# Optimization experiments

Measured on AMD Instinct MI355X. Metric: run time of the kernel, lower is better.

The kernel has to match this reference:

```python
import jax, jax.numpy as jnp
import numpy as np

DIM = 768
HEADS = 12
DIM_HEAD = 64
INNER = HEADS * DIM_HEAD  # 768
B, N = 8, 1024


def layernorm(x, gamma, beta, eps=1e-5):
    mu = jnp.mean(x, axis=-1, keepdims=True)
    var = jnp.var(x, axis=-1, keepdims=True)
    return (x - mu) * jax.lax.rsqrt(var + eps) * gamma + beta


def setup_inputs() -> dict:
    key = jax.random.key(0)
    ks = jax.random.split(key, 12)
    s = lambda fan_in: 1.0 / np.sqrt(fan_in)
    return {
        "x": jax.random.normal(ks[0], (B, N, DIM), dtype=jnp.float32),
        "ln1_g": jnp.ones((DIM,), jnp.float32),
        "ln1_b": jnp.zeros((DIM,), jnp.float32),
        "ln2_g": jnp.ones((DIM,), jnp.float32),
        "ln2_b": jnp.zeros((DIM,), jnp.float32),
        "w_qkv": jax.random.uniform(ks[1], (DIM, 3 * INNER), jnp.float32, -s(DIM), s(DIM)),
        "w_out": jax.random.uniform(ks[2], (INNER, DIM), jnp.float32, -s(INNER), s(INNER)),
        "b_out": jax.random.uniform(ks[3], (DIM,), jnp.float32, -s(INNER), s(INNER)),
        "w_ff1": jax.random.uniform(ks[4], (DIM, 4 * DIM), jnp.float32, -s(DIM), s(DIM)),
        "b_ff1": jax.random.uniform(ks[5], (4 * DIM,), jnp.float32, -s(DIM), s(DIM)),
        "w_ff2": jax.random.uniform(ks[6], (4 * DIM, DIM), jnp.float32, -s(4 * DIM), s(4 * DIM)),
        "b_ff2": jax.random.uniform(ks[7], (DIM,), jnp.float32, -s(4 * DIM), s(4 * DIM)),
    }


def reference(x, ln1_g, ln1_b, ln2_g, ln2_b, w_qkv, w_out, b_out, w_ff1, b_ff1, w_ff2, b_ff2):
    # --- attention sub-block (dropout = identity, eval mode) ---
    residual = x
    h = layernorm(x, ln1_g, ln1_b)
    qkv = h @ w_qkv  # [B, N, 3*INNER]
    q, k, v = jnp.split(qkv, 3, axis=-1)
    # b n (h d) -> b h n d
    reshape = lambda t: t.reshape(B, N, HEADS, DIM_HEAD).transpose(0, 2, 1, 3)
    q, k, v = reshape(q), reshape(k), reshape(v)
    scale = DIM_HEAD ** -0.5
    attn = jnp.einsum('bhnd,bhmd->bhnm', q, k) * scale
    attn = jax.nn.softmax(attn, axis=-1)
    out = jnp.einsum('bhnm,bhmd->bhnd', attn, v)
    out = out.transpose(0, 2, 1, 3).reshape(B, N, INNER)  # b h n d -> b n (h d)
    out = out @ w_out + b_out
    x = residual + out
    # --- FFN sub-block ---
    h2 = layernorm(x, ln2_g, ln2_b)
    ff = jax.nn.gelu(h2 @ w_ff1 + b_ff1, approximate=False) @ w_ff2 + b_ff2
    return x + ff
```

## Files before the change

kernel.cpp:

```cpp
#include <hip/hip_runtime.h>
#include <hip/hip_bf16.h>
#include <math.h>
#include <stdint.h>

#define BATCH 8
#define SEQ   1024
#define DIM   768
#define HEADS 12
#define DHEAD 64
#define TOK   (BATCH*SEQ)
#define INNER 768
#define FFDIM 3072
#define QKVN  2304
#define QKLD  1536

typedef float floatx4 __attribute__((ext_vector_type(4)));
typedef __bf16 bf16x8 __attribute__((ext_vector_type(8)));

__device__ __forceinline__ float b2f(uint16_t u) {
    return __uint_as_float(((uint32_t)u) << 16);
}
__device__ __forceinline__ uint16_t f2b(float f) {
    uint32_t x = __float_as_uint(f);
    x += 0x7fffu + ((x >> 16) & 1u);
    return (uint16_t)(x >> 16);
}
__device__ __forceinline__ uint32_t cvt_pk_bf16(float lo, float hi) {
    uint32_t r;
    asm("v_cvt_pk_bf16_f32 %0, %1, %2" : "=v"(r) : "v"(lo), "v"(hi));
    return r;
}
__device__ __forceinline__ float exp2_fast(float x) {
    float r; asm("v_exp_f32 %0, %1" : "=v"(r) : "v"(x)); return r;
}
__device__ __forceinline__ float rcp_fast(float x) {
    float r; asm("v_rcp_f32 %0, %1" : "=v"(r) : "v"(x)); return r;
}

__device__ __forceinline__ float gelu_exact(float v) {
    float x  = v * 0.70710678f;
    float ax = fabsf(x);
    float t  = rcp_fast(fmaf(0.3275911f, ax, 1.0f));
    float poly = t * fmaf(t, fmaf(t, fmaf(t, fmaf(t, 1.061405429f, -1.453152027f),
                          1.421413741f), -0.284496736f), 0.254829592f);
    float e = 1.0f - poly * exp2_fast(x * x * -1.44269504f);
    float erfv = copysignf(e, x);
    return 0.5f * v * (1.0f + erfv);
}

__global__ __launch_bounds__(256) void transpose_all(
    const float* __restrict__ w_qkv, const float* __restrict__ w_out,
    const float* __restrict__ w_ff1, const float* __restrict__ w_ff2,
    uint16_t* __restrict__ WqT, uint16_t* __restrict__ WoT,
    uint16_t* __restrict__ W1T, uint16_t* __restrict__ W2T)
{
    __shared__ float tile[32][33];
    int bid = blockIdx.x;
    const float* in; uint16_t* outp; int R, C, tx, ty;
    if (bid < 1728)      { in = w_qkv; outp = WqT; R = 768;  C = 2304; tx = bid % 72;            ty = bid / 72; }
    else if (bid < 2304) { int q = bid - 1728; in = w_out; outp = WoT; R = 768;  C = 768;  tx = q % 24; ty = q / 24; }
    else if (bid < 4608) { int q = bid - 2304; in = w_ff1; outp = W1T; R = 768;  C = 3072; tx = q % 96; ty = q / 96; }
    else                 { int q = bid - 4608; in = w_ff2; outp = W2T; R = 3072; C = 768;  tx = q % 24; ty = q / 24; }
    int c0 = tx * 32, r0 = ty * 32;
    int x = threadIdx.x;
    int y = threadIdx.y;
    #pragma unroll
    for (int i = y; i < 32; i += 8)
        tile[i][x] = in[(size_t)(r0 + i) * C + c0 + x];
    __syncthreads();
    #pragma unroll
    for (int i = y; i < 32; i += 8)
        outp[(size_t)(c0 + i) * R + r0 + x] = f2b(tile[x][i]);
}

__global__ __launch_bounds__(256) void ln_naive(
    const float* __restrict__ x, const float* __restrict__ g,
    const float* __restrict__ be, uint16_t* __restrict__ y)
{
    const int lane = threadIdx.x & 63;
    const size_t row = blockIdx.x * 4 + (threadIdx.x >> 6);
    float v[12];
    float s = 0.f, ss = 0.f;
    #pragma unroll
    for (int j = 0; j < 12; j++) {
        int idx = lane + j * 64;
        float f = x[row * DIM + idx];
        v[j] = f; s += f; ss += f * f;
    }
    #pragma unroll
    for (int off = 32; off > 0; off >>= 1) {
        s  += __shfl_xor(s, off);
        ss += __shfl_xor(ss, off);
    }
    const float mu = s * (1.f / DIM);
    const float var = ss * (1.f / DIM) - mu * mu;
    const float rstd = rsqrtf(var + 1e-5f);
    #pragma unroll
    for (int j = 0; j < 12; j++) {
        int idx = lane + j * 64;
        y[row * DIM + idx] = f2b((v[j] - mu) * rstd * g[idx] + be[idx]);
    }
}

template<bool BIAS, bool GELU, bool RES, bool OUTF, bool VSPLIT>
__global__ __launch_bounds__(256) void gemm_bt(
    const uint16_t* __restrict__ A, const uint16_t* __restrict__ Bt,
    void* C, const float* __restrict__ bias, int bias_off,
    const float* res, int N, int K, int lda, int ldbt, int ldc,
    uint16_t* __restrict__ vt)
{
    __shared__ __align__(16) uint16_t a_s[2][128 * 32];
    __shared__ __align__(16) uint16_t b_s[2][128 * 32];
    const int tid = threadIdx.x;
    const int wave = tid >> 6, lane = tid & 63;
    const int wr = wave >> 1, wc = wave & 1;

    const int nwg = gridDim.x * gridDim.y;
    int bid = blockIdx.y * gridDim.x + blockIdx.x;
    if ((nwg & 7) == 0)
        bid = (bid & 7) * (nwg >> 3) + (bid >> 3);
    const int tileM = (bid / gridDim.x) * 128;
    const int tileN = (bid % gridDim.x) * 128;

    floatx4 acc[4][4] = {};

    const int scol = (tid & 3) * 8;
    const int srow = tid >> 2;
    const int lm = lane & 15;
    const int lq = lane >> 4;
    const int kq = lq * 8;

    const uint16_t* Ab0 = A  + (size_t)(tileM + srow) * lda;
    const uint16_t* Ab1 = A  + (size_t)(tileM + 64 + srow) * lda;
    const uint16_t* Bb0 = Bt + (size_t)(tileN + srow) * ldbt;
    const uint16_t* Bb1 = Bt + (size_t)(tileN + 64 + srow) * ldbt;

    const int nt = K >> 5;

    uint4 ar0, ar1, br0, br1;
    ar0 = *(const uint4*)(Ab0 + scol);
    ar1 = *(const uint4*)(Ab1 + scol);
    br0 = *(const uint4*)(Bb0 + scol);
    br1 = *(const uint4*)(Bb1 + scol);
    *(uint4*)&a_s[0][srow * 32 + scol]        = ar0;
    *(uint4*)&a_s[0][(64 + srow) * 32 + scol] = ar1;
    *(uint4*)&b_s[0][srow * 32 + scol]        = br0;
    *(uint4*)&b_s[0][(64 + srow) * 32 + scol] = br1;

    int cur = 0;
    for (int t = 0; t < nt; ++t) {
        __syncthreads();

        if (t + 1 < nt) {
            const int kk = (t + 1) * 32 + scol;
            ar0 = *(const uint4*)(Ab0 + kk);
            ar1 = *(const uint4*)(Ab1 + kk);
            br0 = *(const uint4*)(Bb0 + kk);
            br1 = *(const uint4*)(Bb1 + kk);
        }

        bf16x8 af[4], bfr[4];
        #pragma unroll
        for (int rt = 0; rt < 4; rt++) {
            int r = wr * 64 + rt * 16 + lm;
            af[rt] = *(const bf16x8*)&a_s[cur][r * 32 + kq];
        }
        #pragma unroll
        for (int ntt = 0; ntt < 4; ntt++) {
            int n = wc * 64 + ntt * 16 + lm;
            bfr[ntt] = *(const bf16x8*)&b_s[cur][n * 32 + kq];
        }
        #pragma unroll
        for (int rt = 0; rt < 4; rt++)
            #pragma unroll
            for (int ntt = 0; ntt < 4; ntt++)
                acc[rt][ntt] = __builtin_amdgcn_mfma_f32_16x16x32_bf16(
                    af[rt], bfr[ntt], acc[rt][ntt], 0, 0, 0);

        if (t + 1 < nt) {
            *(uint4*)&a_s[cur ^ 1][srow * 32 + scol]        = ar0;
            *(uint4*)&a_s[cur ^ 1][(64 + srow) * 32 + scol] = ar1;
            *(uint4*)&b_s[cur ^ 1][srow * 32 + scol]        = br0;
            *(uint4*)&b_s[cur ^ 1][(64 + srow) * 32 + scol] = br1;
        }
        cur ^= 1;
    }

    const bool vpath = VSPLIT && (tileN >= 1536);
    #pragma unroll
    for (int rt = 0; rt < 4; rt++) {
        int r0 = tileM + wr * 64 + rt * 16 + lq * 4;
        #pragma unroll
        for (int ntt = 0; ntt < 4; ntt++) {
            int cg = tileN + wc * 64 + ntt * 16 + lm;
            if (vpath) {
                int d = cg - 1536;
                int bb = r0 >> 10, s0 = r0 & 1023;
                uint32_t p0 = (uint32_t)f2b(acc[rt][ntt][0]) | ((uint32_t)f2b(acc[rt][ntt][1]) << 16);
                uint32_t p1 = (uint32_t)f2b(acc[rt][ntt][2]) | ((uint32_t)f2b(acc[rt][ntt][3]) << 16);
                uint2 pk; pk.x = p0; pk.y = p1;
                *(uint2*)&vt[((size_t)bb * 768 + d) * 1024 + s0] = pk;
            } else {
                float bvv = BIAS ? bias[bias_off + cg] : 0.f;
                #pragma unroll
                for (int r = 0; r < 4; r++) {
                    float v = acc[rt][ntt][r] + bvv;
                    if (GELU) v = gelu_exact(v);
                    size_t ci = (size_t)(r0 + r) * ldc + cg;
                    if (RES) v += res[ci];
                    if (OUTF) ((float*)C)[ci] = v;
                    else      ((uint16_t*)C)[ci] = f2b(v);
                }
            }
        }
    }
}

#define KSWZ(row, cb) ((cb) ^ (((row) & 7) << 4))
#define NKT (SEQ / 64)
#define SM_C   0.18033688f
#define SM_THR 11.5416f

__global__ __launch_bounds__(512) void flash_mfma(
    uint16_t* qk, const uint16_t* __restrict__ vt)
{
    __shared__ __align__(16) uint16_t k_s[2][64 * 64];
    __shared__ __align__(16) uint16_t v_s[2][64 * 64];
    __shared__ __align__(16) uint16_t p_s[128 * 64];
    char* k_base = (char*)k_s;
    char* v_base = (char*)v_s;
    char* p_c    = (char*)p_s;

    const int t = threadIdx.x;
    const int wq = t >> 6;
    const int lane = t & 63;
    const int lm = lane & 15;
    const int lq = lane >> 4;

    int flat = blockIdx.x + 8 * (blockIdx.y + 12 * blockIdx.z);
    int nw = (flat & 7) * 96 + (flat >> 3);
    const int b   = nw / 96;
    const int rem = nw - b * 96;
    const int h   = rem >> 3;
    const int qb  = rem & 7;

    const size_t rowbase = (size_t)b * SEQ;
    const int hcol = h * DHEAD;

    bf16x8 qf[2];
    {
        const uint16_t* qp = qk + (rowbase + qb*128 + wq*16 + lm) * QKLD + hcol + lq*8;
        qf[0] = *(const bf16x8*)qp;
        qf[1] = *(const bf16x8*)(qp + 32);
    }

    floatx4 O[4] = {};
    float m_q = -1e30f, l_q = 0.f;

    const int s_row = t >> 3;
    const int s_cb  = (t & 7) * 16;
    const size_t kgbase = (rowbase + s_row) * QKLD + INNER + hcol;
    const size_t vgbase = ((size_t)b * 768 + hcol + s_row) * 1024;

    uint4 kr0, vr0;
    {
        kr0 = *(const uint4*)((const char*)(qk + kgbase) + s_cb);
        vr0 = *(const uint4*)((const char*)(vt + vgbase) + s_cb);
        *(uint4*)&k_base[s_row*128 + KSWZ(s_row, s_cb)] = kr0;
        *(uint4*)&v_base[s_row*128 + KSWZ(s_row, s_cb)] = vr0;
    }

    int cur = 0;
    for (int kt = 0; kt < NKT; ++kt) {
        __syncthreads();

        if (kt + 1 < NKT) {
            kr0 = *(const uint4*)((const char*)(qk + kgbase + (size_t)(kt + 1) * 64 * QKLD) + s_cb);
            vr0 = *(const uint4*)((const char*)(vt + vgbase + (size_t)(kt + 1) * 64) + s_cb);
        }

        const char* k_c = k_base + cur * 8192;
        const char* v_c = v_base + cur * 8192;

        floatx4 S[4];
        __builtin_amdgcn_s_setprio(1);
        #pragma unroll
        for (int nt = 0; nt < 4; nt++) {
            const int row = nt*16 + lm;
            bf16x8 ak0 = *(const bf16x8*)&k_c[row*128 + KSWZ(row, lq*16)];
            bf16x8 ak1 = *(const bf16x8*)&k_c[row*128 + KSWZ(row, 64 + lq*16)];
            floatx4 a = {};
            a = __builtin_amdgcn_mfma_f32_16x16x32_bf16(ak0, qf[0], a, 0, 0, 0);
            a = __builtin_amdgcn_mfma_f32_16x16x32_bf16(ak1, qf[1], a, 0, 0, 0);
            S[nt] = a;
        }
        __builtin_amdgcn_s_setprio(0);

        float m0 = fmaxf(fmaxf(S[0][0], S[0][1]), fmaxf(S[0][2], S[0][3]));
        float m1 = fmaxf(fmaxf(S[1][0], S[1][1]), fmaxf(S[1][2], S[1][3]));
        float m2 = fmaxf(fmaxf(S[2][0], S[2][1]), fmaxf(S[2][2], S[2][3]));
        float m3 = fmaxf(fmaxf(S[3][0], S[3][1]), fmaxf(S[3][2], S[3][3]));
        float mx = fmaxf(fmaxf(m0, m1), fmaxf(m2, m3)) * SM_C;
        mx = fmaxf(mx, __shfl_xor(mx, 16));
        mx = fmaxf(mx, __shfl_xor(mx, 32));

        float mn = m_q;
        if (!__all(mx <= m_q + SM_THR)) {
            mn = fmaxf(m_q, mx);
            float alpha = exp2_fast(m_q - mn);
            m_q = mn;
            l_q *= alpha;
            #pragma unroll
            for (int nt = 0; nt < 4; nt++) {
                O[nt][0] *= alpha; O[nt][1] *= alpha;
                O[nt][2] *= alpha; O[nt][3] *= alpha;
            }
        }

        float p[4][4];
        float sum = 0.f;
        #pragma unroll
        for (int nt = 0; nt < 4; nt++) {
            float p0 = exp2_fast(fmaf(S[nt][0], SM_C, -mn));
            float p1 = exp2_fast(fmaf(S[nt][1], SM_C, -mn));
            float p2 = exp2_fast(fmaf(S[nt][2], SM_C, -mn));
            float p3 = exp2_fast(fmaf(S[nt][3], SM_C, -mn));
            p[nt][0] = p0; p[nt][1] = p1; p[nt][2] = p2; p[nt][3] = p3;
            sum += (p0 + p1) + (p2 + p3);
        }
        sum += __shfl_xor(sum, 16);
        sum += __shfl_xor(sum, 32);
        l_q += sum;

        const int prow = wq*16 + lm;
        #pragma unroll
        for (int nt = 0; nt < 4; nt++) {
            uint2 w;
            w.x = cvt_pk_bf16(p[nt][0], p[nt][1]);
            w.y = cvt_pk_bf16(p[nt][2], p[nt][3]);
            *(uint2*)&p_c[prow*128 + KSWZ(prow, nt*32 + lq*8)] = w;
        }

        __builtin_amdgcn_s_setprio(1);
        #pragma unroll
        for (int ks = 0; ks < 2; ks++) {
            bf16x8 bp = *(const bf16x8*)&p_c[prow*128 + KSWZ(prow, ks*64 + lq*16)];
            #pragma unroll
            for (int nt = 0; nt < 4; nt++) {
                const int vrow = nt*16 + lm;
                bf16x8 av = *(const bf16x8*)&v_c[vrow*128 + KSWZ(vrow, ks*64 + lq*16)];
                O[nt] = __builtin_amdgcn_mfma_f32_16x16x32_bf16(av, bp, O[nt], 0, 0, 0);
            }
        }
        __builtin_amdgcn_s_setprio(0);

        if (kt + 1 < NKT) {
            char* kn = k_base + (cur ^ 1) * 8192;
            char* vn = v_base + (cur ^ 1) * 8192;
            *(uint4*)&kn[s_row*128 + KSWZ(s_row, s_cb)] = kr0;
            *(uint4*)&vn[s_row*128 + KSWZ(s_row, s_cb)] = vr0;
        }
        cur ^= 1;
    }

    const float linv = rcp_fast(l_q);
    uint16_t* dst = qk + (rowbase + qb*128 + wq*16 + lm) * QKLD + hcol;
    #pragma unroll
    for (int nt = 0; nt < 4; nt++) {
        uint2 w;
        w.x = cvt_pk_bf16(O[nt][0] * linv, O[nt][1] * linv);
        w.y = cvt_pk_bf16(O[nt][2] * linv, O[nt][3] * linv);
        *(uint2*)&dst[nt*16 + lq*4] = w;
    }
}

extern "C" void kernel_launch(void* const* d_in, const int* in_sizes, int n_in,
                              void* d_out, int out_size, void* d_ws, size_t ws_size,
                              hipStream_t stream) {
    const float* x      = (const float*)d_in[0];
    const float* ln1_g  = (const float*)d_in[1];
    const float* ln1_b  = (const float*)d_in[2];
    const float* ln2_g  = (const float*)d_in[3];
    const float* ln2_b  = (const float*)d_in[4];
    const float* w_qkv  = (const float*)d_in[5];
    const float* w_out  = (const float*)d_in[6];
    const float* b_out  = (const float*)d_in[7];
    const float* w_ff1  = (const float*)d_in[8];
    const float* b_ff1  = (const float*)d_in[9];
    const float* w_ff2  = (const float*)d_in[10];
    const float* b_ff2  = (const float*)d_in[11];
    float* out = (float*)d_out;

    uint16_t* ws  = (uint16_t*)d_ws;
    uint16_t* qk  = ws;
    uint16_t* ffc = ws;
    uint16_t* vT  = ws + (size_t)12582912;
    uint16_t* h   = ws + (size_t)18874368;
    uint16_t* WqT = ws + (size_t)25165824;
    uint16_t* WoT = ws + (size_t)26935296;
    uint16_t* W1T = ws + (size_t)27525120;
    uint16_t* W2T = ws + (size_t)29884416;

    hipLaunchKernelGGL(transpose_all, dim3(6912), dim3(32, 8), 0, stream,
                       w_qkv, w_out, w_ff1, w_ff2, WqT, WoT, W1T, W2T);

    hipLaunchKernelGGL(ln_naive, dim3(TOK/4), dim3(256), 0, stream, x, ln1_g, ln1_b, h);
    hipLaunchKernelGGL((gemm_bt<false, false, false, false, true>), dim3(QKVN/128, TOK/128), dim3(256), 0, stream,
                       h, WqT, qk, nullptr, 0, nullptr, QKVN, DIM, DIM, DIM, QKLD, vT);
    hipLaunchKernelGGL(flash_mfma, dim3(SEQ/128, HEADS, BATCH), dim3(512), 0, stream, qk, vT);
    hipLaunchKernelGGL((gemm_bt<true, false, true, true, false>), dim3(DIM/128, TOK/128), dim3(256), 0, stream,
                       qk, WoT, out, b_out, 0, x, DIM, INNER, QKLD, DIM, DIM, nullptr);
    hipLaunchKernelGGL(ln_naive, dim3(TOK/4), dim3(256), 0, stream, out, ln2_g, ln2_b, h);
    for (int c = 0; c < 2; c++) {
        hipLaunchKernelGGL((gemm_bt<true, true, false, false, false>), dim3(1536/128, TOK/128), dim3(256), 0, stream,
                           h, W1T + (size_t)c*1536*DIM, ffc, b_ff1, c*1536, nullptr,
                           1536, DIM, DIM, DIM, 1536, nullptr);
        if (c == 0) {
            hipLaunchKernelGGL((gemm_bt<true, false, true, true, false>), dim3(DIM/128, TOK/128), dim3(256), 0, stream,
                               ffc, W2T + (size_t)c*1536, out, b_ff2, 0, out,
                               DIM, 1536, 1536, FFDIM, DIM, nullptr);
        } else {
            hipLaunchKernelGGL((gemm_bt<false, false, true, true, false>), dim3(DIM/128, TOK/128), dim3(256), 0, stream,
                               ffc, W2T + (size_t)c*1536, out, nullptr, 0, out,
                               DIM, 1536, 1536, FFDIM, DIM, nullptr);
        }
    }
}
```

Before: 403.1 us.

## Add 256x256-tile GEMM kernel for QKV and FF1 projections

Introduces a new 512-thread GEMM with 256x256 output tiles, register-prefetched double-buffered LDS, and an XCD-aware block remap. It is used for the QKV projection (including the V-transpose epilogue) and the FF1+GELU GEMMs. Larger tiles raise arithmetic intensity and reduce redundant global loads of A and B. In exchange each thread holds a 128-float accumulator, which raises register pressure and may limit occupancy. The grids also shrink (QKV goes to 288 blocks, FF1 to 192), so the 256 CUs may be unevenly loaded.

Result: slower. 417.3 us (+3.5%).

```diff
diff --git a/kernel.cpp b/kernel.cpp
--- a/kernel.cpp
+++ b/kernel.cpp
@@ -216,6 +216,119 @@
     }
 }
 
+template<bool BIAS, bool GELU, bool VSPLIT>
+__global__ __launch_bounds__(512, 2) void gemm_bt256(
+    const uint16_t* __restrict__ A, const uint16_t* __restrict__ Bt,
+    void* C, const float* __restrict__ bias, int bias_off,
+    int K, int lda, int ldbt, int ldc,
+    uint16_t* __restrict__ vt)
+{
+    __shared__ __align__(16) uint16_t a_s[2][256 * 32];
+    __shared__ __align__(16) uint16_t b_s[2][256 * 32];
+    const int tid = threadIdx.x;
+    const int wave = tid >> 6, lane = tid & 63;
+    const int wr = wave >> 2;
+    const int wc = wave & 3;
+
+    const int nwg = gridDim.x * gridDim.y;
+    int bid = blockIdx.y * gridDim.x + blockIdx.x;
+    if ((nwg & 7) == 0)
+        bid = (bid & 7) * (nwg >> 3) + (bid >> 3);
+    const int tileM = (bid / gridDim.x) * 256;
+    const int tileN = (bid % gridDim.x) * 256;
+
+    floatx4 acc[8][4] = {};
+
+    const int scol = (tid & 3) * 8;
+    const int srow = tid >> 2;
+    const int lm = lane & 15;
+    const int lq = lane >> 4;
+    const int kq = lq * 8;
+
+    const uint16_t* Ab0 = A  + (size_t)(tileM + srow) * lda;
+    const uint16_t* Ab1 = A  + (size_t)(tileM + 128 + srow) * lda;
+    const uint16_t* Bb0 = Bt + (size_t)(tileN + srow) * ldbt;
+    const uint16_t* Bb1 = Bt + (size_t)(tileN + 128 + srow) * ldbt;
+
+    const int nt = K >> 5;
+
+    uint4 ar0, ar1, br0, br1;
+    ar0 = *(const uint4*)(Ab0 + scol);
+    ar1 = *(const uint4*)(Ab1 + scol);
+    br0 = *(const uint4*)(Bb0 + scol);
+    br1 = *(const uint4*)(Bb1 + scol);
+    *(uint4*)&a_s[0][srow * 32 + scol]         = ar0;
+    *(uint4*)&a_s[0][(128 + srow) * 32 + scol] = ar1;
+    *(uint4*)&b_s[0][srow * 32 + scol]         = br0;
+    *(uint4*)&b_s[0][(128 + srow) * 32 + scol] = br1;
+
+    int cur = 0;
+    for (int t = 0; t < nt; ++t) {
+        __syncthreads();
+
+        if (t + 1 < nt) {
+            const int kk = (t + 1) * 32 + scol;
+            ar0 = *(const uint4*)(Ab0 + kk);
+            ar1 = *(const uint4*)(Ab1 + kk);
+            br0 = *(const uint4*)(Bb0 + kk);
+            br1 = *(const uint4*)(Bb1 + kk);
+        }
+
+        bf16x8 af[8], bfr[4];
+        #pragma unroll
+        for (int rt = 0; rt < 8; rt++) {
+            int r = wr * 128 + rt * 16 + lm;
+            af[rt] = *(const bf16x8*)&a_s[cur][r * 32 + kq];
+        }
+        #pragma unroll
+        for (int ntt = 0; ntt < 4; ntt++) {
+            int n = wc * 64 + ntt * 16 + lm;
+            bfr[ntt] = *(const bf16x8*)&b_s[cur][n * 32 + kq];
+        }
+        #pragma unroll
+        for (int rt = 0; rt < 8; rt++)
+            #pragma unroll
+            for (int ntt = 0; ntt < 4; ntt++)
+                acc[rt][ntt] = __builtin_amdgcn_mfma_f32_16x16x32_bf16(
+                    af[rt], bfr[ntt], acc[rt][ntt], 0, 0, 0);
+
+        if (t + 1 < nt) {
+            *(uint4*)&a_s[cur ^ 1][srow * 32 + scol]         = ar0;
+            *(uint4*)&a_s[cur ^ 1][(128 + srow) * 32 + scol] = ar1;
+            *(uint4*)&b_s[cur ^ 1][srow * 32 + scol]         = br0;
+            *(uint4*)&b_s[cur ^ 1][(128 + srow) * 32 + scol] = br1;
+        }
+        cur ^= 1;
+    }
+
+    const bool vpath = VSPLIT && (tileN >= 1536);
+    #pragma unroll
+    for (int rt = 0; rt < 8; rt++) {
+        int r0 = tileM + wr * 128 + rt * 16 + lq * 4;
+        #pragma unroll
+        for (int ntt = 0; ntt < 4; ntt++) {
+            int cg = tileN + wc * 64 + ntt * 16 + lm;
+            if (vpath) {
+                int d = cg - 1536;
+                int bb = r0 >> 10, s0 = r0 & 1023;
+                uint32_t p0 = (uint32_t)f2b(acc[rt][ntt][0]) | ((uint32_t)f2b(acc[rt][ntt][1]) << 16);
+                uint32_t p1 = (uint32_t)f2b(acc[rt][ntt][2]) | ((uint32_t)f2b(acc[rt][ntt][3]) << 16);
+                uint2 pk; pk.x = p0; pk.y = p1;
+                *(uint2*)&vt[((size_t)bb * 768 + d) * 1024 + s0] = pk;
+            } else {
+                float bvv = BIAS ? bias[bias_off + cg] : 0.f;
+                #pragma unroll
+                for (int r = 0; r < 4; r++) {
+                    float v = acc[rt][ntt][r] + bvv;
+                    if (GELU) v = gelu_exact(v);
+                    size_t ci = (size_t)(r0 + r) * ldc + cg;
+                    ((uint16_t*)C)[ci] = f2b(v);
+                }
+            }
+        }
+    }
+}
+
 #define KSWZ(row, cb) ((cb) ^ (((row) & 7) << 4))
 #define NKT (SEQ / 64)
 #define SM_C   0.18033688f
@@ -405,16 +518,16 @@
                        w_qkv, w_out, w_ff1, w_ff2, WqT, WoT, W1T, W2T);
 
     hipLaunchKernelGGL(ln_naive, dim3(TOK/4), dim3(256), 0, stream, x, ln1_g, ln1_b, h);
-    hipLaunchKernelGGL((gemm_bt<false, false, false, false, true>), dim3(QKVN/128, TOK/128), dim3(256), 0, stream,
-                       h, WqT, qk, nullptr, 0, nullptr, QKVN, DIM, DIM, DIM, QKLD, vT);
+    hipLaunchKernelGGL((gemm_bt256<false, false, true>), dim3(QKVN/256, TOK/256), dim3(512), 0, stream,
+                       h, WqT, qk, nullptr, 0, DIM, DIM, DIM, QKLD, vT);
     hipLaunchKernelGGL(flash_mfma, dim3(SEQ/128, HEADS, BATCH), dim3(512), 0, stream, qk, vT);
     hipLaunchKernelGGL((gemm_bt<true, false, true, true, false>), dim3(DIM/128, TOK/128), dim3(256), 0, stream,
                        qk, WoT, out, b_out, 0, x, DIM, INNER, QKLD, DIM, DIM, nullptr);
     hipLaunchKernelGGL(ln_naive, dim3(TOK/4), dim3(256), 0, stream, out, ln2_g, ln2_b, h);
     for (int c = 0; c < 2; c++) {
-        hipLaunchKernelGGL((gemm_bt<true, true, false, false, false>), dim3(1536/128, TOK/128), dim3(256), 0, stream,
-                           h, W1T + (size_t)c*1536*DIM, ffc, b_ff1, c*1536, nullptr,
-                           1536, DIM, DIM, DIM, 1536, nullptr);
+        hipLaunchKernelGGL((gemm_bt256<true, true, false>), dim3(1536/256, TOK/256), dim3(512), 0, stream,
+                           h, W1T + (size_t)c*1536*DIM, ffc, b_ff1, c*1536,
+                           DIM, DIM, DIM, 1536, nullptr);
         if (c == 0) {
             hipLaunchKernelGGL((gemm_bt<true, false, true, true, false>), dim3(DIM/128, TOK/128), dim3(256), 0, stream,
                                ffc, W2T + (size_t)c*1536, out, b_ff2, 0, out,
```
